# Kernel optimization log

Measured on AMD Instinct MI355X. Metric: run time of the kernel, lower is better.

The kernel has to match this reference:

```python
import jax, jax.numpy as jnp
import numpy as np
from jax import lax

K = 4096          # top-k spatial positions kept per (batch, gate-channel)
STRIDE = 4        # conv stride == gating_kernel_size so upsample restores input HxW
GKS = (4, 4)      # gating_kernel_size


def setup_inputs() -> dict:
    key = jax.random.key(0)
    k1, k2 = jax.random.split(key)
    inputs = jax.random.normal(k1, (64, 3, 512, 512), dtype=jnp.float32)
    # torch init.normal_(mean=0, std=1e-4)
    gating_kernel = jax.random.normal(k2, (1, 3, 4, 4), dtype=jnp.float32) * 1e-4
    return {"inputs": inputs, "gating_kernel": gating_kernel}


def reference(inputs, gating_kernel):
    # Small dense conv: [B,3,H,W] -> [B,1,h,w] with h=H/4, w=W/4
    g = lax.conv_general_dilated(
        inputs, gating_kernel,
        window_strides=(STRIDE, STRIDE), padding='VALID',
        dimension_numbers=('NCHW', 'OIHW', 'NCHW'))
    b, c, h, w = g.shape
    gf = g.reshape(b * c, h * w)                      # [B*C, h*w]
    values, idx = lax.top_k(gf, K)                    # [B*C, K] each
    # scatter top-k values back into a zero grid (indices unique per row)
    rows = jnp.arange(b * c)[:, None]
    ret = jnp.zeros_like(gf).at[rows, idx].add(values)
    ret = ret.reshape(b, c, h, w)
    # nearest-neighbor upsample 4x4 and broadcast across the 3 input channels
    ret = jnp.repeat(ret, GKS[0], axis=2)
    ret = jnp.repeat(ret, GKS[1], axis=3)
    ret = jnp.repeat(ret, 3, axis=1)                  # gating_kernel in-channels
    return inputs * ret
```

## Files before the change

### kernel.cpp

```cpp
#include <hip/hip_runtime.h>
#include <hip/hip_bf16.h>

#define B      64
#define CIN    3
#define HW     512
#define OW     128
#define GN     16384
#define ROWS   64
#define KSEL   4096

__global__ __launch_bounds__(256) void conv_kernel(
    const float* __restrict__ in, const float* __restrict__ w,
    double* __restrict__ g) {
  int f = blockIdx.x * 256 + threadIdx.x;
  int ox = f & 127;
  int oy = (f >> 7) & 127;
  int b  = f >> 14;

  const float4* inp = (const float4*)in;
  double acc = 0.0;
#pragma unroll
  for (int c = 0; c < CIN; ++c) {
#pragma unroll
    for (int ky = 0; ky < 4; ++ky) {
      int row = (b * CIN + c) * HW + (4 * oy + ky);
      float4 v = inp[row * (HW / 4) + ox];
      const float* wp = w + (c * 4 + ky) * 4;
      acc = fma((double)v.x, (double)wp[0], acc);
      acc = fma((double)v.y, (double)wp[1], acc);
      acc = fma((double)v.z, (double)wp[2], acc);
      acc = fma((double)v.w, (double)wp[3], acc);
    }
  }
  g[f] = acc;
}

__global__ __launch_bounds__(256) void select_kernel(
    const double* __restrict__ g, float* __restrict__ gsel) {
  const int r = blockIdx.x;
  const int t = threadIdx.x;
  const int base = r * GN;

  unsigned hk[64];
  unsigned lk[64];
#pragma unroll
  for (int j = 0; j < 64; ++j) {
    double d = g[base + t * 64 + j];
    unsigned long long u = (unsigned long long)__double_as_longlong(d);
    u = (u >> 63) ? ~u : (u | 0x8000000000000000ULL);
    hk[j] = (unsigned)(u >> 32);
    lk[j] = (unsigned)u;
  }

  __shared__ int red[4];
  __shared__ int scanbuf[256];

  auto block_reduce = [&](int val) -> int {
#pragma unroll
    for (int o = 32; o > 0; o >>= 1) val += __shfl_down(val, o, 64);
    int wid = t >> 6, lane = t & 63;
    if (lane == 0) red[wid] = val;
    __syncthreads();
    int s = red[0] + red[1] + red[2] + red[3];
    __syncthreads();
    return s;
  };

  unsigned H = 0;
  for (int bit = 31; bit >= 0; --bit) {
    unsigned cand = H | (1u << bit);
    int c = 0;
#pragma unroll
    for (int j = 0; j < 64; ++j) c += (hk[j] >= cand) ? 1 : 0;
    if (block_reduce(c) >= KSEL) H = cand;
  }
  int cgt = 0, ceq = 0;
#pragma unroll
  for (int j = 0; j < 64; ++j) {
    cgt += (hk[j] > H) ? 1 : 0;
    ceq += (hk[j] == H) ? 1 : 0;
  }
  cgt = block_reduce(cgt);
  ceq = block_reduce(ceq);
  int quota = KSEL - cgt;

  bool need_low = (quota < ceq);
  unsigned L = 0;
  int quota2 = 0, ceq2 = 0;
  bool need_rank = false;
  if (need_low) {
    for (int bit = 31; bit >= 0; --bit) {
      unsigned cand = L | (1u << bit);
      int c = 0;
#pragma unroll
      for (int j = 0; j < 64; ++j)
        c += (hk[j] == H && lk[j] >= cand) ? 1 : 0;
      if (block_reduce(c) >= quota) L = cand;
    }
    int cgt2 = 0, ce2 = 0;
#pragma unroll
    for (int j = 0; j < 64; ++j) {
      cgt2 += (hk[j] == H && lk[j] > L) ? 1 : 0;
      ce2  += (hk[j] == H && lk[j] == L) ? 1 : 0;
    }
    cgt2 = block_reduce(cgt2);
    ceq2 = block_reduce(ce2);
    quota2 = quota - cgt2;
    need_rank = (quota2 < ceq2);
  }

  int myoffset = 0;
  if (need_rank) {
    int c = 0;
#pragma unroll
    for (int j = 0; j < 64; ++j) c += (hk[j] == H && lk[j] == L) ? 1 : 0;
    scanbuf[t] = c;
    __syncthreads();
    if (t == 0) {
      int s = 0;
      for (int i = 0; i < 256; ++i) { int x = scanbuf[i]; scanbuf[i] = s; s += x; }
    }
    __syncthreads();
    myoffset = scanbuf[t];
  }

  int seq = 0;
#pragma unroll
  for (int j = 0; j < 64; ++j) {
    bool sel;
    if (hk[j] > H)       sel = true;
    else if (hk[j] < H)  sel = false;
    else if (!need_low)  sel = true;
    else if (lk[j] > L)  sel = true;
    else if (lk[j] < L)  sel = false;
    else if (!need_rank) sel = true;
    else { sel = (myoffset + seq) < quota2; seq++; }

    unsigned long long u = ((unsigned long long)hk[j] << 32) | lk[j];
    unsigned long long bits = (u >> 63) ? (u ^ 0x8000000000000000ULL) : ~u;
    double d = __longlong_as_double((long long)bits);
    gsel[base + t * 64 + j] = sel ? (float)d : 0.0f;
  }
}

__global__ __launch_bounds__(256) void mul_kernel(
    const float4* __restrict__ in, const float* __restrict__ gsel,
    float4* __restrict__ out) {
  unsigned f = blockIdx.x * 256 + threadIdx.x;
  unsigned x4 = f & 127;
  unsigned y  = (f >> 7) & 511;
  unsigned bc = f >> 16;
  unsigned b  = bc / 3u;
  float s = gsel[b * GN + (y >> 2) * OW + x4];
  float4 v = in[f];
  float4 o;
  o.x = v.x * s; o.y = v.y * s; o.z = v.z * s; o.w = v.w * s;
  out[f] = o;
}

extern "C" void kernel_launch(void* const* d_in, const int* in_sizes, int n_in,
                              void* d_out, int out_size, void* d_ws, size_t ws_size,
                              hipStream_t stream) {
  const float* in = (const float*)d_in[0];
  const float* w  = (const float*)d_in[1];
  float* out = (float*)d_out;

  double* g    = (double*)d_ws;
  float*  gsel = (float*)((char*)d_ws + (size_t)ROWS * GN * 8);

  conv_kernel<<<(B * OW * OW) / 256, 256, 0, stream>>>(in, w, g);
  select_kernel<<<ROWS, 256, 0, stream>>>(g, gsel);
  mul_kernel<<<(B * CIN * HW * HW / 4) / 256, 256, 0, stream>>>(
      (const float4*)in, gsel, (float4*)out);
}
```

Measured before the change: 403.6 us.

## Replace bitwise top-k threshold search with radix histogram select; skip zero-gated loads

The selection kernel moves from a 64-step bit-by-bit threshold search with block reductions to a radix-select over 12-bit digits. It uses shared-memory atomic histograms, 1024 threads per row, coalesced strided loads and an early exit once the threshold bin is fully taken. The multiply kernel also skips reading the input when the gate value is zero, which saves about three quarters of the input reads. The costs are shared-atomic contention and a quadratic tie-rank fallback, which should rarely be hit.

```diff
diff --git a/kernel.cpp b/kernel.cpp
--- a/kernel.cpp
+++ b/kernel.cpp
@@ -8,6 +8,9 @@
 #define GN     16384
 #define ROWS   64
 #define KSEL   4096
+
+#define SEL_T  1024
+#define EPT    16
 
 __global__ __launch_bounds__(256) void conv_kernel(
     const float* __restrict__ in, const float* __restrict__ w,
@@ -35,111 +38,119 @@
   g[f] = acc;
 }
 
-__global__ __launch_bounds__(256) void select_kernel(
+__global__ __launch_bounds__(1024) void select_kernel(
     const double* __restrict__ g, float* __restrict__ gsel) {
-  const int r = blockIdx.x;
-  const int t = threadIdx.x;
-  const int base = r * GN;
+  const int r    = blockIdx.x;
+  const int t    = threadIdx.x;
+  const int lane = t & 63;
+  const int wave = t >> 6;
+  const size_t base = (size_t)r * GN;
 
-  unsigned hk[64];
-  unsigned lk[64];
+  unsigned long long k[EPT];
 #pragma unroll
-  for (int j = 0; j < 64; ++j) {
-    double d = g[base + t * 64 + j];
+  for (int j = 0; j < EPT; ++j) {
+    double d = g[base + j * SEL_T + t];
     unsigned long long u = (unsigned long long)__double_as_longlong(d);
-    u = (u >> 63) ? ~u : (u | 0x8000000000000000ULL);
-    hk[j] = (unsigned)(u >> 32);
-    lk[j] = (unsigned)u;
+    k[j] = (u >> 63) ? ~u : (u | 0x8000000000000000ULL);
   }
 
-  __shared__ int red[4];
-  __shared__ int scanbuf[256];
+  __shared__ int hist[4096];
+  __shared__ int wsum[16];
+  __shared__ int sbin, sq, sm;
+  __shared__ int smask[SEL_T];
 
-  auto block_reduce = [&](int val) -> int {
+  unsigned long long P = 0;
+  int shift = 64;
+  int q = KSEL;
+  bool done = false;
+
+  for (int pass = 0; pass < 6 && !done; ++pass) {
+    const int sb = (pass < 5) ? 12 : 4;
+    shift -= sb;
+    const int nb = 1 << sb;
+
+    for (int i = t; i < nb; i += SEL_T) hist[i] = 0;
+    __syncthreads();
+
 #pragma unroll
-    for (int o = 32; o > 0; o >>= 1) val += __shfl_down(val, o, 64);
-    int wid = t >> 6, lane = t & 63;
-    if (lane == 0) red[wid] = val;
+    for (int j = 0; j < EPT; ++j) {
+      bool match = (pass == 0) || ((k[j] >> (shift + sb)) == P);
+      if (match) atomicAdd(&hist[(int)((k[j] >> shift) & (nb - 1))], 1);
+    }
     __syncthreads();
-    int s = red[0] + red[1] + red[2] + red[3];
+
+    if (nb == 4096) {
+      int c0 = hist[4 * t], c1 = hist[4 * t + 1];
+      int c2 = hist[4 * t + 2], c3 = hist[4 * t + 3];
+      int s = c0 + c1 + c2 + c3;
+      int v = s;
+#pragma unroll
+      for (int off = 1; off < 64; off <<= 1) {
+        int u2 = __shfl_down(v, off, 64);
+        if (lane + off < 64) v += u2;
+      }
+      if (lane == 0) wsum[wave] = v;
+      __syncthreads();
+      int wave_above = 0;
+      for (int w2 = wave + 1; w2 < 16; ++w2) wave_above += wsum[w2];
+      int above = wave_above + (v - s);
+      if (above < q && above + c3 >= q) { sbin = 4*t+3; sq = q - above; sm = c3; }
+      above += c3;
+      if (above < q && above + c2 >= q) { sbin = 4*t+2; sq = q - above; sm = c2; }
+      above += c2;
+      if (above < q && above + c1 >= q) { sbin = 4*t+1; sq = q - above; sm = c1; }
+      above += c1;
+      if (above < q && above + c0 >= q) { sbin = 4*t+0; sq = q - above; sm = c0; }
+      __syncthreads();
+    } else {
+      if (t == 0) {
+        int above = 0;
+        for (int bn = nb - 1; bn >= 0; --bn) {
+          int c = hist[bn];
+          if (above < q && above + c >= q) { sbin = bn; sq = q - above; sm = c; break; }
+          above += c;
+        }
+      }
+      __syncthreads();
+    }
+
+    P = (P << sb) | (unsigned long long)sbin;
+    q = sq;
+    if (sq == sm) done = true;
     __syncthreads();
-    return s;
-  };
-
-  unsigned H = 0;
-  for (int bit = 31; bit >= 0; --bit) {
-    unsigned cand = H | (1u << bit);
-    int c = 0;
-#pragma unroll
-    for (int j = 0; j < 64; ++j) c += (hk[j] >= cand) ? 1 : 0;
-    if (block_reduce(c) >= KSEL) H = cand;
-  }
-  int cgt = 0, ceq = 0;
-#pragma unroll
-  for (int j = 0; j < 64; ++j) {
-    cgt += (hk[j] > H) ? 1 : 0;
-    ceq += (hk[j] == H) ? 1 : 0;
-  }
-  cgt = block_reduce(cgt);
-  ceq = block_reduce(ceq);
-  int quota = KSEL - cgt;
-
-  bool need_low = (quota < ceq);
-  unsigned L = 0;
-  int quota2 = 0, ceq2 = 0;
-  bool need_rank = false;
-  if (need_low) {
-    for (int bit = 31; bit >= 0; --bit) {
-      unsigned cand = L | (1u << bit);
-      int c = 0;
-#pragma unroll
-      for (int j = 0; j < 64; ++j)
-        c += (hk[j] == H && lk[j] >= cand) ? 1 : 0;
-      if (block_reduce(c) >= quota) L = cand;
-    }
-    int cgt2 = 0, ce2 = 0;
-#pragma unroll
-    for (int j = 0; j < 64; ++j) {
-      cgt2 += (hk[j] == H && lk[j] > L) ? 1 : 0;
-      ce2  += (hk[j] == H && lk[j] == L) ? 1 : 0;
-    }
-    cgt2 = block_reduce(cgt2);
-    ceq2 = block_reduce(ce2);
-    quota2 = quota - cgt2;
-    need_rank = (quota2 < ceq2);
   }
 
-  int myoffset = 0;
+  const bool need_rank = !done;
   if (need_rank) {
-    int c = 0;
+    int mask = 0;
 #pragma unroll
-    for (int j = 0; j < 64; ++j) c += (hk[j] == H && lk[j] == L) ? 1 : 0;
-    scanbuf[t] = c;
+    for (int j = 0; j < EPT; ++j) if (k[j] == P) mask |= (1 << j);
+    smask[t] = mask;
     __syncthreads();
-    if (t == 0) {
-      int s = 0;
-      for (int i = 0; i < 256; ++i) { int x = scanbuf[i]; scanbuf[i] = s; s += x; }
-    }
-    __syncthreads();
-    myoffset = scanbuf[t];
   }
 
-  int seq = 0;
 #pragma unroll
-  for (int j = 0; j < 64; ++j) {
+  for (int j = 0; j < EPT; ++j) {
     bool sel;
-    if (hk[j] > H)       sel = true;
-    else if (hk[j] < H)  sel = false;
-    else if (!need_low)  sel = true;
-    else if (lk[j] > L)  sel = true;
-    else if (lk[j] < L)  sel = false;
-    else if (!need_rank) sel = true;
-    else { sel = (myoffset + seq) < quota2; seq++; }
-
-    unsigned long long u = ((unsigned long long)hk[j] << 32) | lk[j];
-    unsigned long long bits = (u >> 63) ? (u ^ 0x8000000000000000ULL) : ~u;
+    if (!need_rank) {
+      sel = (k[j] >> shift) >= P;
+    } else {
+      if (k[j] > P)      sel = true;
+      else if (k[j] < P) sel = false;
+      else {
+        int rk = 0;
+        for (int t2 = 0; t2 < SEL_T; ++t2) {
+          int m2 = smask[t2];
+          rk += __popc(m2 & ((1 << j) - 1));
+          if (t2 < t) rk += (m2 >> j) & 1;
+        }
+        sel = rk < q;
+      }
+    }
+    unsigned long long kk = k[j];
+    unsigned long long bits = (kk >> 63) ? (kk ^ 0x8000000000000000ULL) : ~kk;
     double d = __longlong_as_double((long long)bits);
-    gsel[base + t * 64 + j] = sel ? (float)d : 0.0f;
+    gsel[base + j * SEL_T + t] = sel ? (float)d : 0.0f;
   }
 }
 
@@ -152,9 +163,13 @@
   unsigned bc = f >> 16;
   unsigned b  = bc / 3u;
   float s = gsel[b * GN + (y >> 2) * OW + x4];
-  float4 v = in[f];
   float4 o;
-  o.x = v.x * s; o.y = v.y * s; o.z = v.z * s; o.w = v.w * s;
+  if (s != 0.0f) {
+    float4 v = in[f];
+    o.x = v.x * s; o.y = v.y * s; o.z = v.z * s; o.w = v.w * s;
+  } else {
+    o.x = 0.0f; o.y = 0.0f; o.z = 0.0f; o.w = 0.0f;
+  }
   out[f] = o;
 }
 
@@ -169,7 +184,7 @@
   float*  gsel = (float*)((char*)d_ws + (size_t)ROWS * GN * 8);
 
   conv_kernel<<<(B * OW * OW) / 256, 256, 0, stream>>>(in, w, g);
-  select_kernel<<<ROWS, 256, 0, stream>>>(g, gsel);
+  select_kernel<<<ROWS, SEL_T, 0, stream>>>(g, gsel);
   mul_kernel<<<(B * CIN * HW * HW / 4) / 256, 256, 0, stream>>>(
       (const float4*)in, gsel, (float4*)out);
 }
```

Result: faster. 375.5 us, median of 2 (-7.0%).
